# Kernel tuning notes

Measured on AMD Instinct MI355X. Metric: run time of the kernel, lower is better.

## Reference

```python
import jax, jax.numpy as jnp
import numpy as np

PATCH = 8      # patch_size
NFREQ = 8      # fourie_freq


def _fourier_feats(nH, nW, F, dtype):
    # Per-patch positional Fourier features: sin/cos of normalized patch-center
    # coords at F dyadic frequencies for both axes -> [nH, nW, 4F].
    iy = (jnp.arange(nH, dtype=jnp.float32) + 0.5) / nH
    ix = (jnp.arange(nW, dtype=jnp.float32) + 0.5) / nW
    freqs = (2.0 ** jnp.arange(F, dtype=jnp.float32)) * jnp.pi
    fy = iy[:, None] * freqs[None, :]  # [nH, F]
    fx = ix[:, None] * freqs[None, :]  # [nW, F]
    feats = jnp.concatenate([
        jnp.broadcast_to(jnp.sin(fy)[:, None, :], (nH, nW, F)),
        jnp.broadcast_to(jnp.cos(fy)[:, None, :], (nH, nW, F)),
        jnp.broadcast_to(jnp.sin(fx)[None, :, :], (nH, nW, F)),
        jnp.broadcast_to(jnp.cos(fx)[None, :, :], (nH, nW, F)),
    ], axis=-1)
    return feats.astype(dtype)


def setup_inputs() -> dict:
    key = jax.random.key(0)
    ks = jax.random.split(key, 5)
    B, C, H, W = 16, 64, 128, 128
    E, OC, P, F = 8, 64, PATCH, NFREQ
    GC = C + 4 * F  # gate_channel = 96
    x = jax.random.normal(ks[0], (B, C, H, W), jnp.float32)
    expert_w = jax.random.normal(ks[1], (E, OC, C, 3, 3), jnp.float32) * 0.05
    expert_b = jax.random.normal(ks[2], (E, OC), jnp.float32) * 0.05
    gate_w = jax.random.normal(ks[3], (E, GC * P * P), jnp.float32) * 0.02
    gate_b = jnp.zeros((E,), jnp.float32)
    return {"x": x, "expert_w": expert_w, "expert_b": expert_b,
            "gate_w": gate_w, "gate_b": gate_b}


def reference(x, expert_w, expert_b, gate_w, gate_b):
    B, C, H, W = x.shape
    E, OC = expert_w.shape[0], expert_w.shape[1]
    P, F = PATCH, NFREQ
    nH, nW = H // P, W // P

    # --- gating: per-patch softmax over experts ---
    # patches: [B, nH, nW, C, P, P] (matches nn.Flatten over (C,P,P))
    patches = x.reshape(B, C, nH, P, nW, P).transpose(0, 2, 4, 1, 3, 5)
    feats = _fourier_feats(nH, nW, F, x.dtype)                       # [nH,nW,4F]
    pos = jnp.broadcast_to(feats[None, :, :, :, None, None],
                           (B, nH, nW, 4 * F, P, P))
    gate_in = jnp.concatenate([patches, pos], axis=3).reshape(B, nH, nW, -1)
    logits = jnp.einsum('bhwf,ef->bhwe', gate_in, gate_w) + gate_b
    gate = jax.nn.softmax(logits, axis=-1)                           # [B,nH,nW,E]

    # --- experts: all E convs fused into a single conv, then gated combine ---
    wk = expert_w.reshape(E * OC, C, 3, 3)
    y = jax.lax.conv_general_dilated(
        x, wk, window_strides=(1, 1), padding='SAME',
        dimension_numbers=('NCHW', 'OIHW', 'NCHW'))
    y = y + expert_b.reshape(E * OC)[None, :, None, None]
    y = jax.nn.relu(y).reshape(B, E, OC, H, W)

    # upsample per-patch gates to pixel resolution: [B,E,H,W]
    g = gate.transpose(0, 3, 1, 2)                                   # [B,E,nH,nW]
    g = jnp.repeat(jnp.repeat(g, P, axis=2), P, axis=3)
    out = jnp.einsum('behw,bechw->bchw', g, y)                       # [B,OC,H,W]
    return out
```

## Files before the change

kernel.cpp:

```cpp
#include <hip/hip_runtime.h>

typedef short v8s __attribute__((ext_vector_type(8)));
typedef float v4f __attribute__((ext_vector_type(4)));

#define NCH    64
#define NHH    128
#define NWW    128
#define NOC    64
#define KSTEPS 18

#define CSTR 72
#define COLS 66
#define SLAB_BYTES (6 * COLS * CSTR * 2)
#define BBUF_OFF   SLAB_BYTES
#define LDSG_OFF   (SLAB_BYTES + 16384)
#define SMEM_BYTES 73728

__device__ __forceinline__ unsigned short f2bf(float f) {
  unsigned int u = __float_as_uint(f);
  u += 0x7FFFu + ((u >> 16) & 1u);
  return (unsigned short)(u >> 16);
}

__global__ void pack_b_kernel(const float* __restrict__ ew,
                              unsigned short* __restrict__ bp) {
  int f = blockIdx.x * 256 + threadIdx.x;
  int j = f & 7;
  int t = f >> 3;
  int lane = t & 63;
  t >>= 6;
  int nt = t & 3;
  t >>= 2;
  int s = t % KSTEPS;
  int e = t / KSTEPS;
  int k = s * 32 + (lane >> 4) * 8 + j;
  int n = nt * 16 + (lane & 15);
  int khw = k >> 6;
  int c = k & 63;
  bp[f] = f2bf(ew[((e * NOC + n) * NCH + c) * 9 + khw]);
}

__global__ void gate_kernel(const float* __restrict__ x,
                            const float* __restrict__ gw,
                            const float* __restrict__ gb,
                            float* __restrict__ gate_out) {
  int pid = blockIdx.x;
  int pw = pid & 15;
  int ph = (pid >> 4) & 15;
  int b  = pid >> 8;
  int tid = threadIdx.x;

  float cy = (ph + 0.5f) / 16.0f;
  float cx = (pw + 0.5f) / 16.0f;

  float acc[8];
#pragma unroll
  for (int e = 0; e < 8; ++e) acc[e] = 0.f;

  for (int u = tid; u < 1024; u += 256) {
    int ch = u >> 4;
    int pix = (u & 15) * 4;
    int py = pix >> 3;
    int px = pix & 7;
    const float4 xv = *(const float4*)&x[((b * NCH + ch) * NHH + ph * 8 + py) * NWW + pw * 8 + px];
    int fidx = ch * 64 + pix;
#pragma unroll
    for (int e = 0; e < 8; ++e) {
      const float4 wv = *(const float4*)&gw[e * 6144 + fidx];
      acc[e] += xv.x * wv.x + xv.y * wv.y + xv.z * wv.z + xv.w * wv.w;
    }
  }
  for (int u = tid; u < 512; u += 256) {
    int j = u >> 4;
    int g4 = (u & 15) * 4;
    float freq = (float)(1 << (j & 7)) * 3.14159265358979323846f;
    float base = (j < 16) ? cy : cx;
    float a = base * freq;
    float v = ((j >> 3) & 1) ? cosf(a) : sinf(a);
    int fidx = 4096 + j * 64 + g4;
#pragma unroll
    for (int e = 0; e < 8; ++e) {
      const float4 wv = *(const float4*)&gw[e * 6144 + fidx];
      acc[e] += v * (wv.x + wv.y + wv.z + wv.w);
    }
  }

#pragma unroll
  for (int e = 0; e < 8; ++e)
    for (int off = 32; off > 0; off >>= 1)
      acc[e] += __shfl_down(acc[e], off, 64);

  __shared__ float red[8][4];
  int wid = tid >> 6;
  int lane = tid & 63;
  if (lane == 0) {
#pragma unroll
    for (int e = 0; e < 8; ++e) red[e][wid] = acc[e];
  }
  __syncthreads();
  if (tid == 0) {
    float lg[8];
    float mx = -1e30f;
#pragma unroll
    for (int e = 0; e < 8; ++e) {
      lg[e] = red[e][0] + red[e][1] + red[e][2] + red[e][3] + gb[e];
      mx = fmaxf(mx, lg[e]);
    }
    float sum = 0.f;
#pragma unroll
    for (int e = 0; e < 8; ++e) { lg[e] = expf(lg[e] - mx); sum += lg[e]; }
    float inv = 1.0f / sum;
#pragma unroll
    for (int e = 0; e < 8; ++e) gate_out[pid * 8 + e] = lg[e] * inv;
  }
}

__device__ __forceinline__ void load_stage(const unsigned short* __restrict__ bp,
                                           char* smem, int gs, int buf,
                                           int wid, int lane) {
  const char* gsrc = (const char*)bp + gs * 8192 + wid * 2048 + lane * 16;
  char* ldst = smem + BBUF_OFF + buf * 8192 + wid * 2048;
  __builtin_amdgcn_global_load_lds(
      (const __attribute__((address_space(1))) void*)gsrc,
      (__attribute__((address_space(3))) void*)ldst, 16, 0, 0);
  __builtin_amdgcn_global_load_lds(
      (const __attribute__((address_space(1))) void*)(gsrc + 1024),
      (__attribute__((address_space(3))) void*)(ldst + 1024), 16, 0, 0);
}

__global__ __launch_bounds__(256, 2) void moe_conv_kernel(
    const float* __restrict__ x,
    const float* __restrict__ eb,
    const unsigned short* __restrict__ bp,
    const float* __restrict__ gate,
    float* __restrict__ out) {
  __shared__ __align__(16) char smem[SMEM_BYTES];
  unsigned short* slab = (unsigned short*)smem;
  unsigned short* bbufs = (unsigned short*)(smem + BBUF_OFF);
  float* ldsg = (float*)(smem + LDSG_OFF);

  const int tid = threadIdx.x;
  const int bid = blockIdx.x;
  const int wseg = bid & 1;
  const int hq = (bid >> 1) & 31;
  const int b = bid >> 6;
  const int w0 = wseg * 64;
  const int wid = tid >> 6;
  const int lane = tid & 63;
  const int quad = lane >> 4;
  const int l15 = lane & 15;
  const int rp  = wid >> 1;
  const int och = wid & 1;
  const int ntb = och * 2;

  load_stage(bp, smem, 0, 0, wid, lane);

  if (tid < 64) {
    ldsg[tid] = gate[((b * 16 + (hq >> 1)) * 16 + wseg * 8 + (tid >> 3)) * 8 + (tid & 7)];
  }

  const int hbase = hq * 4 - 1;
  const int wbase = w0 - 1;
  for (int flat = tid; flat < 6 * 32 * COLS; flat += 256) {
    int col = flat % COLS;
    int t = flat / COLS;
    int cp = t & 31;
    int r = t >> 5;
    int gh = hbase + r;
    int gw_ = wbase + col;
    float v0 = 0.f, v1 = 0.f;
    if (((unsigned)gh < 128u) && ((unsigned)gw_ < 128u)) {
      const float* px = x + (((b * NCH + cp * 2) * NHH + gh) * NWW + gw_);
      v0 = px[0];
      v1 = px[NHH * NWW];
    }
    unsigned int pk = (unsigned int)f2bf(v0) | ((unsigned int)f2bf(v1) << 16);
    *(unsigned int*)&slab[(r * COLS + col) * CSTR + cp * 2] = pk;
  }
  __syncthreads();

  const v4f vzero = {0.f, 0.f, 0.f, 0.f};
  v4f oacc[8][2];
#pragma unroll
  for (int mt = 0; mt < 8; ++mt) {
    oacc[mt][0] = vzero;
    oacc[mt][1] = vzero;
  }

  const unsigned short* abase = &slab[(rp * 2 * COLS + l15) * CSTR + quad * 8];

  for (int e = 0; e < 8; ++e) {
    v4f vacc[8][2];
#pragma unroll
    for (int mt = 0; mt < 8; ++mt) {
      vacc[mt][0] = vzero;
      vacc[mt][1] = vzero;
    }

#pragma unroll
    for (int st = 0; st < 9; ++st) {
      const int gs = e * 9 + st;
      if (gs > 0) __syncthreads();
      if (gs + 1 < 72) load_stage(bp, smem, gs + 1, (gs + 1) & 1, wid, lane);

      const unsigned short* bstage = bbufs + (gs & 1) * 4096;
#pragma unroll
      for (int sub = 0; sub < 2; ++sub) {
        const int sl = st * 2 + sub;
        const int kh = sl / 6;
        const int kw = (sl / 2) % 3;
        const int ch = sl & 1;
        const v8s b0 = *(const v8s*)(bstage + (sub * 4 + ntb) * 512 + lane * 8);
        const v8s b1 = *(const v8s*)(bstage + (sub * 4 + ntb + 1) * 512 + lane * 8);
#pragma unroll
        for (int mt = 0; mt < 8; ++mt) {
          const v8s a = *(const v8s*)(abase +
              (((mt >> 2) + kh) * COLS + (mt & 3) * 16 + kw) * CSTR + ch * 32);
          vacc[mt][0] = __builtin_amdgcn_mfma_f32_16x16x32_bf16(a, b0, vacc[mt][0], 0, 0, 0);
          vacc[mt][1] = __builtin_amdgcn_mfma_f32_16x16x32_bf16(a, b1, vacc[mt][1], 0, 0, 0);
        }
      }
    }

    float bias0 = eb[e * NOC + ntb * 16 + l15];
    float bias1 = eb[e * NOC + (ntb + 1) * 16 + l15];
#pragma unroll
    for (int mt = 0; mt < 8; ++mt) {
      float g = ldsg[((mt & 3) * 2 + (quad >> 1)) * 8 + e];
#pragma unroll
      for (int r = 0; r < 4; ++r) {
        float v0 = fmaxf(vacc[mt][0][r] + bias0, 0.f);
        float v1 = fmaxf(vacc[mt][1][r] + bias1, 0.f);
        oacc[mt][0][r] += v0 * g;
        oacc[mt][1][r] += v1 * g;
      }
    }
  }

  __syncthreads();
  float* tb = (float*)smem + wid * 4352;
#pragma unroll
  for (int i = 0; i < 2; ++i)
#pragma unroll
    for (int mt = 0; mt < 8; ++mt)
      *(v4f*)(tb + (mt >> 2) * 2176 + (i * 16 + l15) * 68 + (mt & 3) * 16 + quad * 4) =
          oacc[mt][i];

  const int h0 = hq * 4 + rp * 2;
#pragma unroll
  for (int r2 = 0; r2 < 2; ++r2) {
    const int h = h0 + r2;
#pragma unroll
    for (int g4 = 0; g4 < 8; ++g4) {
      const int ocl = g4 * 4 + quad;
      const v4f vv = *(const v4f*)(tb + r2 * 2176 + ocl * 68 + l15 * 4);
      float* dst = out + ((b * NOC + och * 32 + ocl) * NHH + h) * NWW + w0 + l15 * 4;
      *(v4f*)dst = vv;
    }
  }
}

extern "C" void kernel_launch(void* const* d_in, const int* in_sizes, int n_in,
                              void* d_out, int out_size, void* d_ws, size_t ws_size,
                              hipStream_t stream) {
  const float* x  = (const float*)d_in[0];
  const float* ew = (const float*)d_in[1];
  const float* eb = (const float*)d_in[2];
  const float* gw = (const float*)d_in[3];
  const float* gb = (const float*)d_in[4];
  float* out = (float*)d_out;

  unsigned short* bp = (unsigned short*)d_ws;
  float* gate = (float*)((char*)d_ws + 589824);

  hipLaunchKernelGGL(pack_b_kernel, dim3(1152), dim3(256), 0, stream, ew, bp);
  hipLaunchKernelGGL(gate_kernel, dim3(4096), dim3(256), 0, stream, x, gw, gb, gate);
  hipLaunchKernelGGL(moe_conv_kernel, dim3(1024), dim3(256), 0, stream, x, eb, bp, gate, out);
}
```

Measured before the change: 307.4 us.

## Restructure gate kernel to process a patch row per block with LDS reuse

The gating kernel now assigns one block per row of 16 patches instead of one block per patch. It stages x in shared memory and has each wave handle one expert, so gate weights are loaded once and reused across 16 patches. The positional Fourier contribution is folded into precomputed per-feature weight sums. This reduces redundant gate-weight traffic but launches far fewer blocks, which may underfill the GPU.

New measurement: 284.4 us. 7.5% less time.

```diff
diff --git a/kernel.cpp b/kernel.cpp
--- a/kernel.cpp
+++ b/kernel.cpp
@@ -15,6 +15,8 @@
 #define BBUF_OFF   SLAB_BYTES
 #define LDSG_OFF   (SLAB_BYTES + 16384)
 #define SMEM_BYTES 73728
+
+#define GW_STRIDE 6144
 
 __device__ __forceinline__ unsigned short f2bf(float f) {
   unsigned int u = __float_as_uint(f);
@@ -40,78 +42,100 @@
   bp[f] = f2bf(ew[((e * NOC + n) * NCH + c) * 9 + khw]);
 }
 
-__global__ void gate_kernel(const float* __restrict__ x,
-                            const float* __restrict__ gw,
-                            const float* __restrict__ gb,
-                            float* __restrict__ gate_out) {
-  int pid = blockIdx.x;
-  int pw = pid & 15;
-  int ph = (pid >> 4) & 15;
-  int b  = pid >> 8;
-  int tid = threadIdx.x;
-
-  float cy = (ph + 0.5f) / 16.0f;
-  float cx = (pw + 0.5f) / 16.0f;
-
-  float acc[8];
-#pragma unroll
-  for (int e = 0; e < 8; ++e) acc[e] = 0.f;
-
-  for (int u = tid; u < 1024; u += 256) {
-    int ch = u >> 4;
-    int pix = (u & 15) * 4;
-    int py = pix >> 3;
-    int px = pix & 7;
-    const float4 xv = *(const float4*)&x[((b * NCH + ch) * NHH + ph * 8 + py) * NWW + pw * 8 + px];
-    int fidx = ch * 64 + pix;
-#pragma unroll
-    for (int e = 0; e < 8; ++e) {
-      const float4 wv = *(const float4*)&gw[e * 6144 + fidx];
-      acc[e] += xv.x * wv.x + xv.y * wv.y + xv.z * wv.z + xv.w * wv.w;
-    }
-  }
-  for (int u = tid; u < 512; u += 256) {
-    int j = u >> 4;
-    int g4 = (u & 15) * 4;
-    float freq = (float)(1 << (j & 7)) * 3.14159265358979323846f;
-    float base = (j < 16) ? cy : cx;
-    float a = base * freq;
-    float v = ((j >> 3) & 1) ? cosf(a) : sinf(a);
-    int fidx = 4096 + j * 64 + g4;
-#pragma unroll
-    for (int e = 0; e < 8; ++e) {
-      const float4 wv = *(const float4*)&gw[e * 6144 + fidx];
-      acc[e] += v * (wv.x + wv.y + wv.z + wv.w);
-    }
-  }
-
-#pragma unroll
-  for (int e = 0; e < 8; ++e)
-    for (int off = 32; off > 0; off >>= 1)
-      acc[e] += __shfl_down(acc[e], off, 64);
-
-  __shared__ float red[8][4];
-  int wid = tid >> 6;
-  int lane = tid & 63;
-  if (lane == 0) {
-#pragma unroll
-    for (int e = 0; e < 8; ++e) red[e][wid] = acc[e];
+__global__ __launch_bounds__(512) void gate_kernel(
+    const float* __restrict__ x,
+    const float* __restrict__ gw,
+    const float* __restrict__ gb,
+    float* __restrict__ gate_out) {
+  __shared__ float xs[16][8][132];
+  __shared__ float wsum[8][32];
+  __shared__ float lg[16][8];
+
+  const int pid = blockIdx.x;
+  const int ph = pid & 15;
+  const int b = pid >> 4;
+  const int tid = threadIdx.x;
+  const int e = tid >> 6;
+  const int lane = tid & 63;
+
+  if (tid < 256) {
+    int e2 = tid >> 5, j = tid & 31;
+    const float* p = gw + e2 * GW_STRIDE + 4096 + j * 64;
+    float s = 0.f;
+#pragma unroll
+    for (int g = 0; g < 16; ++g) {
+      float4 v = *(const float4*)(p + g * 4);
+      s += v.x + v.y + v.z + v.w;
+    }
+    wsum[e2][j] = s;
+  }
+
+  float acc[16];
+#pragma unroll
+  for (int pw = 0; pw < 16; ++pw) acc[pw] = 0.f;
+
+  const float* xrow = x + ((size_t)(b * NCH) * NHH + ph * 8) * NWW;
+
+  for (int cc = 0; cc < 4; ++cc) {
+    __syncthreads();
+    for (int i = tid; i < 4096; i += 512) {
+      int c = i >> 8;
+      int py = (i >> 5) & 7;
+      int w4 = i & 31;
+      float4 v = *(const float4*)&xrow[(cc * 16 + c) * (NHH * NWW) + py * NWW + w4 * 4];
+      *(float4*)&xs[c][py][w4 * 4] = v;
+    }
+    __syncthreads();
+#pragma unroll
+    for (int i = 0; i < 4; ++i) {
+      int g = lane + 64 * i;
+      int pxg = g & 1;
+      int py = (g >> 1) & 7;
+      int c = g >> 4;
+      const float4 wv = *(const float4*)&gw[e * GW_STRIDE + (cc * 16 + c) * 64 + py * 8 + pxg * 4];
+      const float* xp = &xs[c][py][pxg * 4];
+#pragma unroll
+      for (int pw = 0; pw < 16; ++pw) {
+        float4 xv = *(const float4*)(xp + pw * 8);
+        acc[pw] += xv.x * wv.x + xv.y * wv.y + xv.z * wv.z + xv.w * wv.w;
+      }
+    }
+  }
+
+#pragma unroll
+  for (int pw = 0; pw < 16; ++pw) {
+    float v = acc[pw];
+#pragma unroll
+    for (int off = 32; off > 0; off >>= 1) v += __shfl_xor(v, off, 64);
+    if (lane == 0) lg[pw][e] = v;
   }
   __syncthreads();
-  if (tid == 0) {
-    float lg[8];
+
+  if (tid < 16) {
+    const int pw = tid;
+    const float cy = (ph + 0.5f) / 16.0f;
+    const float cx = (pw + 0.5f) / 16.0f;
+    float l[8];
+#pragma unroll
+    for (int ee = 0; ee < 8; ++ee) l[ee] = lg[pw][ee] + gb[ee];
+    for (int j = 0; j < 32; ++j) {
+      float freq = (float)(1 << (j & 7)) * 3.14159265358979323846f;
+      float base = (j < 16) ? cy : cx;
+      float a = base * freq;
+      float v = ((j >> 3) & 1) ? cosf(a) : sinf(a);
+#pragma unroll
+      for (int ee = 0; ee < 8; ++ee) l[ee] += v * wsum[ee][j];
+    }
     float mx = -1e30f;
 #pragma unroll
-    for (int e = 0; e < 8; ++e) {
-      lg[e] = red[e][0] + red[e][1] + red[e][2] + red[e][3] + gb[e];
-      mx = fmaxf(mx, lg[e]);
-    }
+    for (int ee = 0; ee < 8; ++ee) mx = fmaxf(mx, l[ee]);
     float sum = 0.f;
 #pragma unroll
-    for (int e = 0; e < 8; ++e) { lg[e] = expf(lg[e] - mx); sum += lg[e]; }
+    for (int ee = 0; ee < 8; ++ee) { l[ee] = expf(l[ee] - mx); sum += l[ee]; }
     float inv = 1.0f / sum;
 #pragma unroll
-    for (int e = 0; e < 8; ++e) gate_out[pid * 8 + e] = lg[e] * inv;
+    for (int ee = 0; ee < 8; ++ee)
+      gate_out[(pid * 16 + pw) * 8 + ee] = l[ee] * inv;
   }
 }
 
@@ -274,6 +298,6 @@
   float* gate = (float*)((char*)d_ws + 589824);
 
   hipLaunchKernelGGL(pack_b_kernel, dim3(1152), dim3(256), 0, stream, ew, bp);
-  hipLaunchKernelGGL(gate_kernel, dim3(4096), dim3(256), 0, stream, x, gw, gb, gate);
+  hipLaunchKernelGGL(gate_kernel, dim3(256), dim3(512), 0, stream, x, gw, gb, gate);
   hipLaunchKernelGGL(moe_conv_kernel, dim3(1024), dim3(256), 0, stream, x, eb, bp, gate, out);
 }
```
